# Kernel optimization log

Hardware: AMD Instinct MI355X
Metric: run time of the kernel (lower is better)

The kernel has to match this reference:

```python
import jax, jax.numpy as jnp
import numpy as np

N = 100000      # nodes
E = 1600000     # edges (avg degree 16)
D_IN = 128
D_OUT = 128
ORDER = 2
EPS = 1e-9


def setup_inputs() -> dict:
    key = jax.random.key(0)
    ks = jax.random.split(key, 8)
    inp = {}
    inp["vecs"] = jax.random.normal(ks[0], (N, D_IN), dtype=jnp.float32)
    inp["adj_vals"] = jax.random.uniform(ks[1], (E,), dtype=jnp.float32)
    inp["row"] = jax.random.randint(ks[2], (E,), 0, N)
    inp["col"] = jax.random.randint(ks[3], (E,), 0, N)
    lim = float(np.sqrt(6.0 / (D_IN + D_OUT)))  # glorot uniform
    for o in range(ORDER + 1):
        inp[f"W{o}"] = jax.random.uniform(ks[4 + o], (D_IN, D_OUT), dtype=jnp.float32, minval=-lim, maxval=lim)
        inp[f"b{o}"] = jnp.zeros((D_OUT,), jnp.float32)
        inp[f"off{o}"] = jnp.zeros((1, D_OUT), jnp.float32)
        inp[f"sc{o}"] = jnp.ones((1, D_OUT), jnp.float32)
    return inp


def _spmm(vals, row, col, x):
    # sparse_tensor_dense_matmul: out[r] = sum_e vals[e] * x[col[e]] for row[e]==r
    return jax.ops.segment_sum(vals[:, None] * x[col], row, num_segments=N)


def _f_nonlinear(v, W, b, off, sc):
    vw = jax.nn.relu(v @ W + b)
    mean = jnp.mean(vw, axis=1, keepdims=True)
    var = jnp.var(vw, axis=1, keepdims=True)
    # tf.nn.batch_normalization with per-row moments, eps=1e-9
    return sc * (vw - mean) * jax.lax.rsqrt(var + EPS) + off


def reference(vecs, adj_vals, row, col,
              W0, W1, W2, b0, b1, b2,
              off0, off1, off2, sc0, sc1, sc2):
    Ws = [W0, W1, W2]
    bs = [b0, b1, b2]
    offs = [off0, off1, off2]
    scs = [sc0, sc1, sc2]
    # vecs_hop[k] = A^k @ vecs (dropout=0 -> identity)
    hops = [vecs]
    for _ in range(ORDER):
        hops.append(_spmm(adj_vals, row, col, hops[-1]))
    outs = [_f_nonlinear(hops[o], Ws[o], bs[o], offs[o], scs[o]) for o in range(ORDER + 1)]
    ret = outs[0]
    for o in range(1, ORDER + 1):  # aggr == 'mean' (actually a sum in the source)
        ret = ret + outs[o]
    return ret
```

## Files before the change

kernel.cpp:

```cpp
#include <hip/hip_runtime.h>
#include <math.h>

#define NN 100000
#define DD 128
#define NB 391
#define RP_PAD 100004

typedef short bf16x8 __attribute__((ext_vector_type(8)));
typedef float f32x4  __attribute__((ext_vector_type(4)));
typedef unsigned uint4v __attribute__((ext_vector_type(4)));

__device__ __forceinline__ unsigned f2bf_rne(float f) {
    unsigned u = __float_as_uint(f);
    return (u + 0x7FFFu + ((u >> 16) & 1u)) >> 16;
}
__device__ __forceinline__ unsigned packbf(float a, float b) {
    return f2bf_rne(a) | (f2bf_rne(b) << 16);
}
__device__ __forceinline__ float bf_lo(unsigned u) { return __uint_as_float(u << 16); }
__device__ __forceinline__ float bf_hi(unsigned u) { return __uint_as_float(u & 0xFFFF0000u); }

__device__ __forceinline__ int2 ldnt_edge(const int2* p) {
    long long v = __builtin_nontemporal_load((const long long*)p);
    int2 r;
    r.x = (int)(v & 0xffffffffll);
    r.y = (int)(((unsigned long long)v) >> 32);
    return r;
}

__global__ __launch_bounds__(256) void bucket_scatter(
    const int* __restrict__ row, const int* __restrict__ col,
    const float* __restrict__ vals, int* __restrict__ bcnt,
    int2* __restrict__ ep_raw, int E, int CAP)
{
    __shared__ int cnt[NB];
    __shared__ int base[NB];
    for (int j = threadIdx.x; j < NB; j += 256) cnt[j] = 0;
    __syncthreads();
    int cb = blockIdx.x * 8192;
    int ce = min(cb + 8192, E);
    for (int j = cb + threadIdx.x; j < ce; j += 256)
        atomicAdd(&cnt[row[j] >> 8], 1);
    __syncthreads();
    for (int j = threadIdx.x; j < NB; j += 256) {
        int c = cnt[j];
        base[j] = c ? (j * CAP + atomicAdd(&bcnt[j], c)) : 0;
        cnt[j] = 0;
    }
    __syncthreads();
    for (int j = cb + threadIdx.x; j < ce; j += 256) {
        int r = row[j];
        int c = __builtin_nontemporal_load(col + j);
        float v = __builtin_nontemporal_load(vals + j);
        int b = r >> 8;
        int off = atomicAdd(&cnt[b], 1);
        unsigned meta = (unsigned)c | ((unsigned)(r & 255) << 17);
        ep_raw[base[b] + off] = make_int2((int)meta, __float_as_int(v));
    }
}

__global__ __launch_bounds__(256) void csr_finish_convert(
    const int* __restrict__ bcnt, const int2* __restrict__ ep_raw,
    int* __restrict__ row_ptr, int2* __restrict__ ep,
    const float* __restrict__ vecs, unsigned short* __restrict__ vecs_bf,
    const float* __restrict__ W0, const float* __restrict__ W1,
    const float* __restrict__ W2, unsigned short* __restrict__ Wt,
    int CAP, int N, int E, int n8)
{
    const int b = blockIdx.x;
    const int t = threadIdx.x;

    if (b >= NB) {
        if (b < NB + 24) {
            const int b2 = b - NB;
            const float* W = (b2 < 8) ? W0 : ((b2 < 16) ? W1 : W2);
            unsigned short* dst = Wt + (b2 >> 3) * DD * DD;
            int idx = (b2 & 7) * 256 + t;
            int n = idx >> 4;
            int kc = (idx & 15) * 8;
            unsigned r[4];
            #pragma unroll
            for (int j = 0; j < 4; j++) {
                float a = W[(kc + 2 * j) * DD + n];
                float c = W[(kc + 2 * j + 1) * DD + n];
                r[j] = packbf(a, c);
            }
            *(uint4*)(dst + n * DD + kc) = make_uint4(r[0], r[1], r[2], r[3]);
        } else {
            int i = (b - NB - 24) * 256 + t;
            if (i >= n8) return;
            f32x4 a = __builtin_nontemporal_load((const f32x4*)vecs + (size_t)i * 2);
            f32x4 c = __builtin_nontemporal_load((const f32x4*)vecs + (size_t)i * 2 + 1);
            uint4v o;
            o.x = packbf(a.x, a.y); o.y = packbf(a.z, a.w);
            o.z = packbf(c.x, c.y); o.w = packbf(c.z, c.w);
            ((uint4v*)vecs_bf)[i] = o;
        }
        return;
    }

    __shared__ int red[256];
    __shared__ int rcnt[256];
    __shared__ int rcur[256];
    __shared__ int wsum[4];

    int part = 0;
    for (int j = t; j < b; j += 256) part += bcnt[j];
    red[t] = part;
    __syncthreads();
    #pragma unroll
    for (int off = 128; off > 0; off >>= 1) {
        if (t < off) red[t] += red[t + off];
        __syncthreads();
    }
    const int dst = red[0];
    const int cnt = bcnt[b];
    const int src = b * CAP;

    rcnt[t] = 0;
    __syncthreads();
    for (int j = t; j < cnt; j += 256)
        atomicAdd(&rcnt[(unsigned)ep_raw[src + j].x >> 17], 1);
    __syncthreads();

    int v = rcnt[t];
    int lane = t & 63;
    int inc = v;
    #pragma unroll
    for (int off = 1; off < 64; off <<= 1) {
        int u = __shfl_up(inc, off, 64);
        if (lane >= off) inc += u;
    }
    if (lane == 63) wsum[t >> 6] = inc;
    __syncthreads();
    int woff = 0;
    for (int i = 0; i < (t >> 6); i++) woff += wsum[i];
    int excl = woff + inc - v;

    int grow = b * 256 + t;
    if (grow < N) row_ptr[grow] = dst + excl;
    rcur[t] = excl;
    __syncthreads();

    for (int j = t; j < cnt; j += 256) {
        int2 rec = ldnt_edge(ep_raw + src + j);
        unsigned meta = (unsigned)rec.x;
        int rlo = meta >> 17;
        int c = (int)(meta & 0x1FFFFu);
        int p = atomicAdd(&rcur[rlo], 1);
        ep[dst + p] = make_int2(c, rec.y);
    }
    if (b == 0 && t == 0) row_ptr[N] = E;
}

__device__ __forceinline__ void accum8(float* acc, uint4 u, float v) {
    acc[0] += v * bf_lo(u.x); acc[1] += v * bf_hi(u.x);
    acc[2] += v * bf_lo(u.y); acc[3] += v * bf_hi(u.y);
    acc[4] += v * bf_lo(u.z); acc[5] += v * bf_hi(u.z);
    acc[6] += v * bf_lo(u.w); acc[7] += v * bf_hi(u.w);
}

__global__ __launch_bounds__(256) void spmm_bf16(
    const uint4* __restrict__ x, const int* __restrict__ row_ptr,
    const int2* __restrict__ ep, uint4* __restrict__ out, int N)
{
    int t = blockIdx.x * 256 + threadIdx.x;
    int g = t >> 4;
    int lane = t & 15;
    if (g >= N) return;

    int s = row_ptr[g];
    int e = row_ptr[g + 1];
    float acc[8] = {0.f, 0.f, 0.f, 0.f, 0.f, 0.f, 0.f, 0.f};

    int k = s;
    for (; k + 8 <= e; k += 8) {
        int2 E0 = ep[k + 0], E1 = ep[k + 1], E2 = ep[k + 2], E3 = ep[k + 3];
        int2 E4 = ep[k + 4], E5 = ep[k + 5], E6 = ep[k + 6], E7 = ep[k + 7];
        uint4 X0 = x[(size_t)E0.x * 16 + lane];
        uint4 X1 = x[(size_t)E1.x * 16 + lane];
        uint4 X2 = x[(size_t)E2.x * 16 + lane];
        uint4 X3 = x[(size_t)E3.x * 16 + lane];
        uint4 X4 = x[(size_t)E4.x * 16 + lane];
        uint4 X5 = x[(size_t)E5.x * 16 + lane];
        uint4 X6 = x[(size_t)E6.x * 16 + lane];
        uint4 X7 = x[(size_t)E7.x * 16 + lane];
        accum8(acc, X0, __int_as_float(E0.y));
        accum8(acc, X1, __int_as_float(E1.y));
        accum8(acc, X2, __int_as_float(E2.y));
        accum8(acc, X3, __int_as_float(E3.y));
        accum8(acc, X4, __int_as_float(E4.y));
        accum8(acc, X5, __int_as_float(E5.y));
        accum8(acc, X6, __int_as_float(E6.y));
        accum8(acc, X7, __int_as_float(E7.y));
    }
    for (; k + 4 <= e; k += 4) {
        int2 E0 = ep[k + 0], E1 = ep[k + 1], E2 = ep[k + 2], E3 = ep[k + 3];
        uint4 X0 = x[(size_t)E0.x * 16 + lane];
        uint4 X1 = x[(size_t)E1.x * 16 + lane];
        uint4 X2 = x[(size_t)E2.x * 16 + lane];
        uint4 X3 = x[(size_t)E3.x * 16 + lane];
        accum8(acc, X0, __int_as_float(E0.y));
        accum8(acc, X1, __int_as_float(E1.y));
        accum8(acc, X2, __int_as_float(E2.y));
        accum8(acc, X3, __int_as_float(E3.y));
    }
    for (; k < e; k++) {
        int2 E0 = ep[k];
        uint4 X0 = x[(size_t)E0.x * 16 + lane];
        accum8(acc, X0, __int_as_float(E0.y));
    }

    uint4 o;
    o.x = packbf(acc[0], acc[1]); o.y = packbf(acc[2], acc[3]);
    o.z = packbf(acc[4], acc[5]); o.w = packbf(acc[6], acc[7]);
    out[(size_t)g * 16 + lane] = o;
}

__device__ __forceinline__ void bn_accum(
    f32x4* acc, const float* __restrict__ bias, const float* __restrict__ off,
    const float* __restrict__ sc, int i, float facc[8][4])
{
    float bc[8], sv[8], ov[8];
    #pragma unroll
    for (int ct = 0; ct < 8; ct++) {
        int c = ct * 16 + i;
        bc[ct] = bias[c]; sv[ct] = sc[c]; ov[ct] = off[c];
    }
    float s[4] = {0.f, 0.f, 0.f, 0.f};
    float qq[4] = {0.f, 0.f, 0.f, 0.f};
    #pragma unroll
    for (int ct = 0; ct < 8; ct++) {
        #pragma unroll
        for (int r = 0; r < 4; r++) {
            float v = fmaxf(acc[ct][r] + bc[ct], 0.f);
            acc[ct][r] = v;
            s[r] += v;
            qq[r] += v * v;
        }
    }
    #pragma unroll
    for (int r = 0; r < 4; r++) {
        #pragma unroll
        for (int m = 1; m <= 8; m <<= 1) {
            s[r]  += __shfl_xor(s[r],  m, 64);
            qq[r] += __shfl_xor(qq[r], m, 64);
        }
    }
    #pragma unroll
    for (int r = 0; r < 4; r++) {
        float mn = s[r] * 0.0078125f;
        float var = qq[r] * 0.0078125f - mn * mn;
        float rs = rsqrtf(var + 1e-9f);
        #pragma unroll
        for (int ct = 0; ct < 8; ct++)
            facc[ct][r] += sv[ct] * (acc[ct][r] - mn) * rs + ov[ct];
    }
}

__global__ __launch_bounds__(256) void fused_dense_mfma(
    const unsigned short* __restrict__ h0,
    const unsigned short* __restrict__ h1,
    const unsigned short* __restrict__ h2,
    const unsigned short* __restrict__ Wt,
    const float* __restrict__ b0, const float* __restrict__ b1,
    const float* __restrict__ b2,
    const float* __restrict__ off0, const float* __restrict__ off1,
    const float* __restrict__ off2,
    const float* __restrict__ sc0, const float* __restrict__ sc1,
    const float* __restrict__ sc2,
    float* __restrict__ out, int N)
{
    __shared__ uint4 Bl[2048];

    const int tid  = threadIdx.x;
    const int wave = tid >> 6;
    const int lane = tid & 63;
    const int i    = lane & 15;
    const int q    = lane >> 4;
    const int slab = blockIdx.x * 64 + wave * 16;

    int arow = slab + i;
    if (arow >= N) arow = N - 1;

    const unsigned short* hops[3] = {h0, h1, h2};
    const float* bs[3]  = {b0, b1, b2};
    const float* ofs[3] = {off0, off1, off2};
    const float* scs[3] = {sc0, sc1, sc2};
    const bf16x8* Bv = (const bf16x8*)Bl;

    float facc[8][4];
    #pragma unroll
    for (int ct = 0; ct < 8; ct++)
        #pragma unroll
        for (int r = 0; r < 4; r++) facc[ct][r] = 0.f;

    for (int o = 0; o < 3; o++) {
        const uint4* Wg = (const uint4*)(Wt + o * DD * DD);
        #pragma unroll
        for (int j = 0; j < 8; j++) {
            int c  = j * 256 + tid;
            int nn = c & 127;
            int kc = c >> 7;
            Bl[kc * 128 + nn] = Wg[nn * 16 + kc];
        }
        __syncthreads();

        const unsigned short* arow_p = hops[o] + (size_t)arow * DD + q * 8;
        f32x4 acc[8];
        #pragma unroll
        for (int ct = 0; ct < 8; ct++) acc[ct] = (f32x4){0.f, 0.f, 0.f, 0.f};
        #pragma unroll
        for (int kb = 0; kb < 4; kb++) {
            bf16x8 a = __builtin_nontemporal_load((const bf16x8*)(arow_p + kb * 32));
            const int kc = kb * 4 + q;
            #pragma unroll
            for (int ct = 0; ct < 8; ct++) {
                bf16x8 b = Bv[kc * 128 + ct * 16 + i];
                acc[ct] = __builtin_amdgcn_mfma_f32_16x16x32_bf16(a, b, acc[ct], 0, 0, 0);
            }
        }
        bn_accum(acc, bs[o], ofs[o], scs[o], i, facc);
        __syncthreads();
    }

    #pragma unroll
    for (int r = 0; r < 4; r++) {
        int orow = slab + q * 4 + r;
        if (orow < N) {
            float* op = out + (size_t)orow * DD + i;
            #pragma unroll
            for (int ct = 0; ct < 8; ct++)
                __builtin_nontemporal_store(facc[ct][r], op + ct * 16);
        }
    }
}

extern "C" void kernel_launch(void* const* d_in, const int* in_sizes, int n_in,
                              void* d_out, int out_size, void* d_ws, size_t ws_size,
                              hipStream_t stream)
{
    const float* vecs = (const float*)d_in[0];
    const float* adj  = (const float*)d_in[1];
    const int*   row  = (const int*)d_in[2];
    const int*   col  = (const int*)d_in[3];
    const float* W0   = (const float*)d_in[4];
    const float* b0   = (const float*)d_in[5];
    const float* off0 = (const float*)d_in[6];
    const float* sc0  = (const float*)d_in[7];
    const float* W1   = (const float*)d_in[8];
    const float* b1   = (const float*)d_in[9];
    const float* off1 = (const float*)d_in[10];
    const float* sc1  = (const float*)d_in[11];
    const float* W2   = (const float*)d_in[12];
    const float* b2   = (const float*)d_in[13];
    const float* off2 = (const float*)d_in[14];
    const float* sc2  = (const float*)d_in[15];

    const int E = in_sizes[1];
    const int N = NN;

    const int avg = (E + NB - 1) / NB;
    const int CAP = (avg + 8 * (int)sqrt((double)avg) + 79) & ~15;

    unsigned short* hop1_bf = (unsigned short*)d_ws;
    unsigned short* hop2_bf = hop1_bf + (size_t)N * DD;
    unsigned short* vecs_bf = hop2_bf + (size_t)N * DD;
    unsigned short* Wt_bf   = vecs_bf + (size_t)N * DD;
    int*   row_ptr  = (int*)(Wt_bf + 3 * DD * DD);
    int*   bcnt     = row_ptr + RP_PAD;
    int2*  ep_raw   = (int2*)(bcnt + 512);
    int2*  epack    = ep_raw + (size_t)NB * CAP;

    hipMemsetAsync(bcnt, 0, NB * sizeof(int), stream);

    const int cb = (E + 8191) / 8192;
    bucket_scatter<<<cb, 256, 0, stream>>>(row, col, adj, bcnt, ep_raw, E, CAP);

    const int n8 = N * DD / 8;
    const int vb = (n8 + 255) / 256;
    csr_finish_convert<<<NB + 24 + vb, 256, 0, stream>>>(
        bcnt, ep_raw, row_ptr, epack,
        vecs, vecs_bf, W0, W1, W2, Wt_bf,
        CAP, N, E, n8);

    int sb = (N * 16 + 255) / 256;
    spmm_bf16<<<sb, 256, 0, stream>>>(
        (const uint4*)vecs_bf, row_ptr, epack, (uint4*)hop1_bf, N);
    spmm_bf16<<<sb, 256, 0, stream>>>(
        (const uint4*)hop1_bf, row_ptr, epack, (uint4*)hop2_bf, N);

    const int db = (N + 63) / 64;
    fused_dense_mfma<<<db, 256, 0, stream>>>(
        vecs_bf, hop1_bf, hop2_bf, Wt_bf,
        b0, b1, b2, off0, off1, off2, sc0, sc1, sc2,
        (float*)d_out, N);
}
```

Measured before the change: 356.0 us.

## Build CSR via global row histogram, scan, and direct atomic scatter

Replaces the two-pass bucketed CSR build (bucket scatter into a padded staging buffer, then per-bucket local sort) with a global per-row histogram using global atomics, a row-pointer scan kernel, and a direct edge scatter driven by global atomic cursors. This drops the intermediate staging buffer and one full read-write pass over the edges. In exchange it adds a kernel launch, a larger memset, and heavy contention-prone global atomics on random rows. The scan kernel also rereads prefix counts quadratically across blocks. Edge order within a row becomes nondeterministic.

```diff
diff --git a/kernel.cpp b/kernel.cpp
--- a/kernel.cpp
+++ b/kernel.cpp
@@ -5,6 +5,7 @@
 #define DD 128
 #define NB 391
 #define RP_PAD 100004
+#define RC_PAD 100352
 
 typedef short bf16x8 __attribute__((ext_vector_type(8)));
 typedef float f32x4  __attribute__((ext_vector_type(4)));
@@ -20,92 +21,60 @@
 __device__ __forceinline__ float bf_lo(unsigned u) { return __uint_as_float(u << 16); }
 __device__ __forceinline__ float bf_hi(unsigned u) { return __uint_as_float(u & 0xFFFF0000u); }
 
-__device__ __forceinline__ int2 ldnt_edge(const int2* p) {
-    long long v = __builtin_nontemporal_load((const long long*)p);
-    int2 r;
-    r.x = (int)(v & 0xffffffffll);
-    r.y = (int)(((unsigned long long)v) >> 32);
-    return r;
-}
-
-__global__ __launch_bounds__(256) void bucket_scatter(
-    const int* __restrict__ row, const int* __restrict__ col,
-    const float* __restrict__ vals, int* __restrict__ bcnt,
-    int2* __restrict__ ep_raw, int E, int CAP)
-{
-    __shared__ int cnt[NB];
-    __shared__ int base[NB];
-    for (int j = threadIdx.x; j < NB; j += 256) cnt[j] = 0;
-    __syncthreads();
-    int cb = blockIdx.x * 8192;
-    int ce = min(cb + 8192, E);
-    for (int j = cb + threadIdx.x; j < ce; j += 256)
-        atomicAdd(&cnt[row[j] >> 8], 1);
-    __syncthreads();
-    for (int j = threadIdx.x; j < NB; j += 256) {
-        int c = cnt[j];
-        base[j] = c ? (j * CAP + atomicAdd(&bcnt[j], c)) : 0;
-        cnt[j] = 0;
-    }
-    __syncthreads();
-    for (int j = cb + threadIdx.x; j < ce; j += 256) {
-        int r = row[j];
-        int c = __builtin_nontemporal_load(col + j);
-        float v = __builtin_nontemporal_load(vals + j);
-        int b = r >> 8;
-        int off = atomicAdd(&cnt[b], 1);
-        unsigned meta = (unsigned)c | ((unsigned)(r & 255) << 17);
-        ep_raw[base[b] + off] = make_int2((int)meta, __float_as_int(v));
-    }
-}
-
-__global__ __launch_bounds__(256) void csr_finish_convert(
-    const int* __restrict__ bcnt, const int2* __restrict__ ep_raw,
-    int* __restrict__ row_ptr, int2* __restrict__ ep,
+__global__ __launch_bounds__(256) void hist_convert(
+    const int* __restrict__ row, int* __restrict__ rcnt,
     const float* __restrict__ vecs, unsigned short* __restrict__ vecs_bf,
     const float* __restrict__ W0, const float* __restrict__ W1,
     const float* __restrict__ W2, unsigned short* __restrict__ Wt,
-    int CAP, int N, int E, int n8)
+    int E, int n8, int hb)
 {
     const int b = blockIdx.x;
     const int t = threadIdx.x;
-
-    if (b >= NB) {
-        if (b < NB + 24) {
-            const int b2 = b - NB;
-            const float* W = (b2 < 8) ? W0 : ((b2 < 16) ? W1 : W2);
-            unsigned short* dst = Wt + (b2 >> 3) * DD * DD;
-            int idx = (b2 & 7) * 256 + t;
-            int n = idx >> 4;
-            int kc = (idx & 15) * 8;
-            unsigned r[4];
-            #pragma unroll
-            for (int j = 0; j < 4; j++) {
-                float a = W[(kc + 2 * j) * DD + n];
-                float c = W[(kc + 2 * j + 1) * DD + n];
-                r[j] = packbf(a, c);
-            }
-            *(uint4*)(dst + n * DD + kc) = make_uint4(r[0], r[1], r[2], r[3]);
-        } else {
-            int i = (b - NB - 24) * 256 + t;
-            if (i >= n8) return;
-            f32x4 a = __builtin_nontemporal_load((const f32x4*)vecs + (size_t)i * 2);
-            f32x4 c = __builtin_nontemporal_load((const f32x4*)vecs + (size_t)i * 2 + 1);
-            uint4v o;
-            o.x = packbf(a.x, a.y); o.y = packbf(a.z, a.w);
-            o.z = packbf(c.x, c.y); o.w = packbf(c.z, c.w);
-            ((uint4v*)vecs_bf)[i] = o;
-        }
-        return;
-    }
-
+    if (b < hb) {
+        int cb = b * 8192;
+        int ce = min(cb + 8192, E);
+        for (int j = cb + t; j < ce; j += 256) {
+            int r = __builtin_nontemporal_load(row + j);
+            atomicAdd(&rcnt[r], 1);
+        }
+    } else if (b < hb + 24) {
+        const int b2 = b - hb;
+        const float* W = (b2 < 8) ? W0 : ((b2 < 16) ? W1 : W2);
+        unsigned short* dst = Wt + (b2 >> 3) * DD * DD;
+        int idx = (b2 & 7) * 256 + t;
+        int n = idx >> 4;
+        int kc = (idx & 15) * 8;
+        unsigned r[4];
+        #pragma unroll
+        for (int j = 0; j < 4; j++) {
+            float a = W[(kc + 2 * j) * DD + n];
+            float c = W[(kc + 2 * j + 1) * DD + n];
+            r[j] = packbf(a, c);
+        }
+        *(uint4*)(dst + n * DD + kc) = make_uint4(r[0], r[1], r[2], r[3]);
+    } else {
+        int i = (b - hb - 24) * 256 + t;
+        if (i >= n8) return;
+        f32x4 a = __builtin_nontemporal_load((const f32x4*)vecs + (size_t)i * 2);
+        f32x4 c = __builtin_nontemporal_load((const f32x4*)vecs + (size_t)i * 2 + 1);
+        uint4v o;
+        o.x = packbf(a.x, a.y); o.y = packbf(a.z, a.w);
+        o.z = packbf(c.x, c.y); o.w = packbf(c.z, c.w);
+        ((uint4v*)vecs_bf)[i] = o;
+    }
+}
+
+__global__ __launch_bounds__(256) void rowptr_scan(
+    const int* __restrict__ rcnt, int* __restrict__ row_ptr,
+    int* __restrict__ rcur, int N, int E)
+{
     __shared__ int red[256];
-    __shared__ int rcnt[256];
-    __shared__ int rcur[256];
     __shared__ int wsum[4];
+    const int b = blockIdx.x;
+    const int t = threadIdx.x;
 
     int part = 0;
-    for (int j = t; j < b; j += 256) part += bcnt[j];
+    for (int j = t; j < b * 256; j += 256) part += rcnt[j];
     red[t] = part;
     __syncthreads();
     #pragma unroll
@@ -113,17 +82,10 @@
         if (t < off) red[t] += red[t + off];
         __syncthreads();
     }
-    const int dst = red[0];
-    const int cnt = bcnt[b];
-    const int src = b * CAP;
-
-    rcnt[t] = 0;
-    __syncthreads();
-    for (int j = t; j < cnt; j += 256)
-        atomicAdd(&rcnt[(unsigned)ep_raw[src + j].x >> 17], 1);
-    __syncthreads();
-
-    int v = rcnt[t];
+    const int base = red[0];
+
+    const int grow = b * 256 + t;
+    int v = (grow < N) ? rcnt[grow] : 0;
     int lane = t & 63;
     int inc = v;
     #pragma unroll
@@ -137,20 +99,28 @@
     for (int i = 0; i < (t >> 6); i++) woff += wsum[i];
     int excl = woff + inc - v;
 
-    int grow = b * 256 + t;
-    if (grow < N) row_ptr[grow] = dst + excl;
-    rcur[t] = excl;
-    __syncthreads();
-
-    for (int j = t; j < cnt; j += 256) {
-        int2 rec = ldnt_edge(ep_raw + src + j);
-        unsigned meta = (unsigned)rec.x;
-        int rlo = meta >> 17;
-        int c = (int)(meta & 0x1FFFFu);
-        int p = atomicAdd(&rcur[rlo], 1);
-        ep[dst + p] = make_int2(c, rec.y);
-    }
-    if (b == 0 && t == 0) row_ptr[N] = E;
+    if (grow < N) {
+        int rp = base + excl;
+        row_ptr[grow] = rp;
+        rcur[grow] = rp;
+    }
+    if (b == NB - 1 && t == 255) row_ptr[N] = base + excl + v;
+}
+
+__global__ __launch_bounds__(256) void edge_scatter(
+    const int* __restrict__ row, const int* __restrict__ col,
+    const float* __restrict__ vals, int* __restrict__ rcur,
+    int2* __restrict__ ep, int E)
+{
+    int cb = blockIdx.x * 2048;
+    int ce = min(cb + 2048, E);
+    for (int j = cb + threadIdx.x; j < ce; j += 256) {
+        int r = __builtin_nontemporal_load(row + j);
+        int c = __builtin_nontemporal_load(col + j);
+        float v = __builtin_nontemporal_load(vals + j);
+        int p = atomicAdd(&rcur[r], 1);
+        ep[p] = make_int2(c, __float_as_int(v));
+    }
 }
 
 __device__ __forceinline__ void accum8(float* acc, uint4 u, float v) {
@@ -360,29 +330,27 @@
     const int E = in_sizes[1];
     const int N = NN;
 
-    const int avg = (E + NB - 1) / NB;
-    const int CAP = (avg + 8 * (int)sqrt((double)avg) + 79) & ~15;
-
     unsigned short* hop1_bf = (unsigned short*)d_ws;
     unsigned short* hop2_bf = hop1_bf + (size_t)N * DD;
     unsigned short* vecs_bf = hop2_bf + (size_t)N * DD;
     unsigned short* Wt_bf   = vecs_bf + (size_t)N * DD;
     int*   row_ptr  = (int*)(Wt_bf + 3 * DD * DD);
-    int*   bcnt     = row_ptr + RP_PAD;
-    int2*  ep_raw   = (int2*)(bcnt + 512);
-    int2*  epack    = ep_raw + (size_t)NB * CAP;
-
-    hipMemsetAsync(bcnt, 0, NB * sizeof(int), stream);
-
-    const int cb = (E + 8191) / 8192;
-    bucket_scatter<<<cb, 256, 0, stream>>>(row, col, adj, bcnt, ep_raw, E, CAP);
-
+    int*   rcnt     = row_ptr + RP_PAD;
+    int*   rcur     = rcnt + RC_PAD;
+    int2*  epack    = (int2*)(rcur + RC_PAD);
+
+    hipMemsetAsync(rcnt, 0, RC_PAD * sizeof(int), stream);
+
+    const int hb = (E + 8191) / 8192;
     const int n8 = N * DD / 8;
     const int vb = (n8 + 255) / 256;
-    csr_finish_convert<<<NB + 24 + vb, 256, 0, stream>>>(
-        bcnt, ep_raw, row_ptr, epack,
-        vecs, vecs_bf, W0, W1, W2, Wt_bf,
-        CAP, N, E, n8);
+    hist_convert<<<hb + 24 + vb, 256, 0, stream>>>(
+        row, rcnt, vecs, vecs_bf, W0, W1, W2, Wt_bf, E, n8, hb);
+
+    rowptr_scan<<<NB, 256, 0, stream>>>(rcnt, row_ptr, rcur, N, E);
+
+    edge_scatter<<<(E + 2047) / 2048, 256, 0, stream>>>(
+        row, col, adj, rcur, epack, E);
 
     int sb = (N * 16 + 255) / 256;
     spmm_bf16<<<sb, 256, 0, stream>>>(
```

Result: slower. 506.5 us (+42.3%).
